# Optimization experiments

Hardware: AMD Instinct MI355X
Metric: run time of the kernel (lower is better)

## Reference

```python
import jax, jax.numpy as jnp
import numpy as np

BS, N, HID = 16384, 16, 512  # batch, n coords (state dim = 2n), mlp hidden


def setup_inputs() -> dict:
    key = jax.random.key(0)
    ks = jax.random.split(key, 4)
    d = 2 * N
    x = jax.random.normal(ks[0], (BS, d), dtype=jnp.float32)
    # Lagrangian MLP: 2n -> HID -> HID -> 1 with softplus (smooth 2nd derivs)
    W1 = jax.random.normal(ks[1], (d, HID), dtype=jnp.float32) / np.sqrt(d)
    b1 = jnp.zeros((HID,), jnp.float32)
    W2 = jax.random.normal(ks[2], (HID, HID), dtype=jnp.float32) / np.sqrt(HID)
    b2 = jnp.zeros((HID,), jnp.float32)
    W3 = jax.random.normal(ks[3], (HID, 1), dtype=jnp.float32) / np.sqrt(HID)
    b3 = jnp.zeros((1,), jnp.float32)
    return {"x": x, "W1": W1, "b1": b1, "W2": W2, "b2": b2, "W3": W3, "b3": b3}


def reference(x, W1, b1, W2, b2, W3, b3):
    n = x.shape[1] // 2

    def lagrangian(qqd):  # qqd: [2n] -> scalar
        h = jax.nn.softplus(qqd @ W1 + b1)
        h = jax.nn.softplus(h @ W2 + b2)
        return jnp.sum(h @ W3 + b3)

    # batched first derivative (jacobian of scalar) and hessian; replaces the
    # per-sample python loop of torch.autograd.functional.jacobian/hessian
    jac = jax.vmap(jax.grad(lagrangian))(x)          # [bs, 2n]
    hess = jax.vmap(jax.hessian(lagrangian))(x)      # [bs, 2n, 2n]

    qd = x[:, n:]                                    # [bs, n]
    A = hess[:, n:, n:]                              # d2L/dqd dqd  [bs, n, n]
    B = hess[:, n:, :n]                              # d2L/dqd dq   [bs, n, n]
    rhs = jac[:, :n] - jnp.einsum('bij,bj->bi', B, qd)  # [bs, n]
    qdd = jnp.einsum('bij,bj->bi', jnp.linalg.pinv(A), rhs)  # [bs, n]
    return jnp.concatenate([qd, qdd], axis=1)        # [bs, 2n]
```

## Files before the change

### kernel.cpp

```cpp
#include <hip/hip_runtime.h>
#include <math.h>


#define NSWEEP 5
#define JAX_RCOND 1.9073486e-5

typedef unsigned int uint;
typedef unsigned short ushort;
typedef float f2 __attribute__((ext_vector_type(2)));
typedef float f4 __attribute__((ext_vector_type(4)));
typedef short bf16x8 __attribute__((ext_vector_type(8)));
typedef float f32x16 __attribute__((ext_vector_type(16)));
typedef uint uint2v __attribute__((ext_vector_type(2)));

#define OFF_R    0
#define R_FLOATS 12288
#define OFF_S1   12288
#define OFF_H1   13312
#define OFF_G2   14336
#define OFF_D2   15360
#define OFF_U    16384
#define OFF_X    17408
#define OFF_JAC  17472
#define OFF_T1   17504
#define OFF_T2   18560
#define OFF_AUG  19616
#define SMEM_FLOATS 20160
#define SMEM_BYTES  (SMEM_FLOATS*4)

#define SOLVE_WAVE_DBL 592
#define SOLVE_SMEM_BYTES (4*SOLVE_WAVE_DBL*8)

#define PACK_BYTES 524288

__device__ __forceinline__ ushort f2bf(float x) {
    uint u = __float_as_uint(x);
    return (ushort)((u + 0x7fffu + ((u >> 16) & 1u)) >> 16);
}
__device__ __forceinline__ float bf2f(ushort h) {
    return __uint_as_float(((uint)h) << 16);
}
__device__ __forceinline__ void split3(float x, ushort& h, ushort& m, ushort& l) {
    h = f2bf(x); float r1 = x - bf2f(h);
    m = f2bf(r1); float r2 = r1 - bf2f(m);
    l = f2bf(r2);
}

__device__ __forceinline__ void pairpq(int r, int m, int& p, int& q) {
    p = (m == 0) ? 0 : 1 + (m - 1 + r) % 15;
    q = 1 + (14 - m + r) % 15;
}

__device__ __forceinline__ void wave_fence() {
    __builtin_amdgcn_wave_barrier();
    __builtin_amdgcn_s_waitcnt(0);
    __builtin_amdgcn_wave_barrier();
}

__device__ __forceinline__ void jacobi_solve_wave(
    const float* __restrict__ gaug, double* __restrict__ ws,
    float* __restrict__ outp, int lane)
{
    double* Ad  = ws;
    double* Vd  = Ad + 272;
    double* c8  = Vd + 272;
    double* sn8 = c8 + 8;
    double* il  = sn8 + 8;
    double* yv  = il + 16;

    for (int idx = lane; idx < 272; idx += 64) {
        const int r = idx / 17, c = idx - r*17;
        double a = 0.0;
        if (c < 16) a = 0.5 * ((double)gaug[r*17 + c] + (double)gaug[c*17 + r]);
        Ad[idx] = a;
        Vd[idx] = (c < 16 && r == c) ? 1.0 : 0.0;
    }
    wave_fence();

    for (int sweep = 0; sweep < NSWEEP; ++sweep) {
        for (int rr = 0; rr < 15; ++rr) {
            if (lane < 8) {
                int p, q; pairpq(rr, lane, p, q);
                const double app = Ad[p*17 + p], aqq = Ad[q*17 + q], apq = Ad[p*17 + q];
                double cc = 1.0, ss = 0.0;
                if (apq != 0.0) {
                    const double tau = (aqq - app) / (2.0 * apq);
                    const double tt = ((tau >= 0.0) ? 1.0 : -1.0) / (fabs(tau) + sqrt(1.0 + tau*tau));
                    cc = 1.0 / sqrt(1.0 + tt*tt);
                    ss = tt * cc;
                }
                c8[lane] = cc; sn8[lane] = ss;
            }
            wave_fence();
            #pragma unroll
            for (int k = 0; k < 2; ++k) {
                const int id = lane + 64*k;
                const int m = id >> 4, j = id & 15;
                int p, q; pairpq(rr, m, p, q);
                const double cc = c8[m], ss = sn8[m];
                const double ap = Ad[p*17 + j], aq = Ad[q*17 + j];
                Ad[p*17 + j] = cc*ap - ss*aq;
                Ad[q*17 + j] = ss*ap + cc*aq;
            }
            #pragma unroll
            for (int k = 0; k < 2; ++k) {
                const int id = lane + 64*k;
                const int m = id >> 4, i = id & 15;
                int p, q; pairpq(rr, m, p, q);
                const double cc = c8[m], ss = sn8[m];
                const double vp = Vd[i*17 + p], vq = Vd[i*17 + q];
                Vd[i*17 + p] = cc*vp - ss*vq;
                Vd[i*17 + q] = ss*vp + cc*vq;
            }
            wave_fence();
            #pragma unroll
            for (int k = 0; k < 2; ++k) {
                const int id = lane + 64*k;
                const int m = id >> 4, i = id & 15;
                int p, q; pairpq(rr, m, p, q);
                const double cc = c8[m], ss = sn8[m];
                const double ap = Ad[i*17 + p], aq = Ad[i*17 + q];
                Ad[i*17 + p] = cc*ap - ss*aq;
                Ad[i*17 + q] = ss*ap + cc*aq;
            }
            wave_fence();
        }
    }

    if (lane == 0) {
        double mx = 0.0;
        #pragma unroll
        for (int i = 0; i < 16; ++i) mx = fmax(mx, fabs(Ad[i*17 + i]));
        const double cut = JAX_RCOND * mx;
        #pragma unroll
        for (int i = 0; i < 16; ++i) {
            const double l = Ad[i*17 + i];
            il[i] = (fabs(l) > cut) ? (1.0 / l) : 0.0;
        }
    }
    wave_fence();

    if (lane < 16) {
        double a = 0.0;
        #pragma unroll
        for (int r = 0; r < 16; ++r) a += Vd[r*17 + lane] * (double)gaug[r*17 + 16];
        yv[lane] = a;
    }
    wave_fence();

    if (lane < 16) {
        double a = 0.0;
        #pragma unroll
        for (int i = 0; i < 16; ++i) a += Vd[lane*17 + i] * (il[i] * yv[i]);
        outp[lane] = (float)a;
    }
}

extern "C" __global__ void w1_transpose(const float* __restrict__ W1,
                                        float* __restrict__ W1T) {
    const int t = blockIdx.x * 256 + threadIdx.x;
    W1T[t] = W1[(t & 31) * 512 + (t >> 5)];
}

extern "C" __global__ void w2_pack(const float* __restrict__ W2,
                                   uint* __restrict__ pHi,
                                   uint* __restrict__ pMid,
                                   uint* __restrict__ pLo) {
    const int tid = blockIdx.x * 256 + threadIdx.x;
    const int lane = tid & 63;
    const int k0 = ((tid >> 6) & 31) * 16 + (lane >> 5) * 8;
    const int n  = (tid >> 11) * 32 + (lane & 31);
    uint h[4], m[4], l[4];
    #pragma unroll
    for (int e2 = 0; e2 < 4; ++e2) {
        ushort h0, m0, l0, h1, m1, l1;
        split3(W2[(k0 + 2*e2    )*512 + n], h0, m0, l0);
        split3(W2[(k0 + 2*e2 + 1)*512 + n], h1, m1, l1);
        h[e2] = (uint)h0 | ((uint)h1 << 16);
        m[e2] = (uint)m0 | ((uint)m1 << 16);
        l[e2] = (uint)l0 | ((uint)l1 << 16);
    }
    #pragma unroll
    for (int e2 = 0; e2 < 4; ++e2) {
        pHi [tid*4 + e2] = h[e2];
        pMid[tid*4 + e2] = m[e2];
        pLo [tid*4 + e2] = l[e2];
    }
}

#define MFMA32(A, B, C) __builtin_amdgcn_mfma_f32_32x32x16_bf16((A), (B), (C), 0, 0, 0)

extern "C" __global__ __launch_bounds__(256, 2)
void lnn_kernel(const float* __restrict__ x,
                const float* __restrict__ W1,
                const float* __restrict__ W1T,
                const float* __restrict__ b1,
                const float* __restrict__ W2, const float* __restrict__ b2,
                const float* __restrict__ W3,
                float* __restrict__ out,
                float* __restrict__ aug_g,
                const uint* __restrict__ pHi,
                const uint* __restrict__ pMid,
                const uint* __restrict__ pLo,
                const int solveInMain)
{
    const int b0 = blockIdx.x * 2;
    const int t = threadIdx.x;
    const int lane = t & 63;
    const int w = t >> 6;

    extern __shared__ float sm[];
    char*  A8    = (char*)sm;
    float* s_ws  = sm + OFF_R;
    char*  Mq8   = (char*)sm;
    float* s_s1  = sm + OFF_S1;
    float* s_h1  = sm + OFF_H1;
    float* s_g2  = sm + OFF_G2;
    float* s_d2  = sm + OFF_D2;
    float* s_u   = sm + OFF_U;
    float* s_x   = sm + OFF_X;
    float* s_jac = sm + OFF_JAC;
    float* s_T1  = sm + OFF_T1;
    float* s_T2  = sm + OFF_T2;
    float* s_aug = sm + OFF_AUG;

    if (t < 64) s_x[t] = x[b0*32 + t];
    if (t < 32) {
        const int s = t >> 4, i = t & 15;
        out[(b0+s)*32 + i] = x[(b0+s)*32 + 16 + i];
    }
    __syncthreads();

    #pragma unroll
    for (int rep = 0; rep < 4; ++rep) {
        const int s = rep >> 1;
        const int j = t + (rep & 1)*256;
        float z = b1[j];
        const f4* wt = (const f4*)(W1T + j*32);
        const float* xs = s_x + s*32;
        #pragma unroll
        for (int i4 = 0; i4 < 8; ++i4) {
            const f4 wv = wt[i4];
            z = fmaf(xs[i4*4 + 0], wv.x, z);
            z = fmaf(xs[i4*4 + 1], wv.y, z);
            z = fmaf(xs[i4*4 + 2], wv.z, z);
            z = fmaf(xs[i4*4 + 3], wv.w, z);
        }
        const float e = expf(-fabsf(z));
        const float sg = (z >= 0.f) ? 1.f/(1.f+e) : e/(1.f+e);
        s_s1[s*512 + j] = sg;
        s_h1[s*512 + j] = fmaxf(z, 0.f) + log1pf(e);
    }
    __syncthreads();

    {
        const int c = w*128 + lane*2;
        const f2 bz = *(const f2*)(b2 + c);
        float za[2][2] = { {bz.x, bz.y}, {bz.x, bz.y} };
        #pragma unroll 8
        for (int j = 0; j < 512; ++j) {
            const f2 wv = *(const f2*)(W2 + j*512 + c);
            const float h0 = s_h1[j];
            const float h1 = s_h1[512 + j];
            za[0][0] = fmaf(h0, wv.x, za[0][0]);
            za[0][1] = fmaf(h0, wv.y, za[0][1]);
            za[1][0] = fmaf(h1, wv.x, za[1][0]);
            za[1][1] = fmaf(h1, wv.y, za[1][1]);
        }
        const f2 w3v = *(const f2*)(W3 + c);
        #pragma unroll
        for (int s = 0; s < 2; ++s) {
            const float e0 = expf(-fabsf(za[s][0]));
            const float sg0 = (za[s][0] >= 0.f) ? 1.f/(1.f+e0) : e0/(1.f+e0);
            const float e1v = expf(-fabsf(za[s][1]));
            const float sg1 = (za[s][1] >= 0.f) ? 1.f/(1.f+e1v) : e1v/(1.f+e1v);
            f2 g2v = { w3v.x * sg0, w3v.y * sg1 };
            f2 d2v = { w3v.x * sg0 * (1.f - sg0), w3v.y * sg1 * (1.f - sg1) };
            *(f2*)(s_g2 + s*512 + c) = g2v;
            *(f2*)(s_d2 + s*512 + c) = d2v;
        }
    }
    __syncthreads();

    {
        float g2a[8], g2b[8];
        {
            const float4 ga = *(const float4*)(s_g2 + lane*8);
            const float4 gb = *(const float4*)(s_g2 + lane*8 + 4);
            g2a[0]=ga.x; g2a[1]=ga.y; g2a[2]=ga.z; g2a[3]=ga.w;
            g2a[4]=gb.x; g2a[5]=gb.y; g2a[6]=gb.z; g2a[7]=gb.w;
            const float4 gc = *(const float4*)(s_g2 + 512 + lane*8);
            const float4 gd = *(const float4*)(s_g2 + 512 + lane*8 + 4);
            g2b[0]=gc.x; g2b[1]=gc.y; g2b[2]=gc.z; g2b[3]=gc.w;
            g2b[4]=gd.x; g2b[5]=gd.y; g2b[6]=gd.z; g2b[7]=gd.w;
        }
        for (int jj = 0; jj < 32; ++jj) {
            float pr0[4], pr1[4];
            #pragma unroll
            for (int s4 = 0; s4 < 4; ++s4) {
                const int j = w*128 + jj + s4*32;
                const float4 ra = *(const float4*)(W2 + j*512 + lane*8);
                const float4 rb = *(const float4*)(W2 + j*512 + lane*8 + 4);
                float p0 = ra.x*g2a[0];
                p0 = fmaf(ra.y, g2a[1], p0); p0 = fmaf(ra.z, g2a[2], p0); p0 = fmaf(ra.w, g2a[3], p0);
                p0 = fmaf(rb.x, g2a[4], p0); p0 = fmaf(rb.y, g2a[5], p0);
                p0 = fmaf(rb.z, g2a[6], p0); p0 = fmaf(rb.w, g2a[7], p0);
                pr0[s4] = p0;
                float p1 = ra.x*g2b[0];
                p1 = fmaf(ra.y, g2b[1], p1); p1 = fmaf(ra.z, g2b[2], p1); p1 = fmaf(ra.w, g2b[3], p1);
                p1 = fmaf(rb.x, g2b[4], p1); p1 = fmaf(rb.y, g2b[5], p1);
                p1 = fmaf(rb.z, g2b[6], p1); p1 = fmaf(rb.w, g2b[7], p1);
                pr1[s4] = p1;
            }
            #pragma unroll
            for (int off = 32; off >= 1; off >>= 1) {
                #pragma unroll
                for (int s4 = 0; s4 < 4; ++s4) {
                    pr0[s4] += __shfl_xor(pr0[s4], off);
                    pr1[s4] += __shfl_xor(pr1[s4], off);
                }
            }
            if (lane == 0) {
                #pragma unroll
                for (int s4 = 0; s4 < 4; ++s4) {
                    s_u[w*128 + jj + s4*32]       = pr0[s4];
                    s_u[512 + w*128 + jj + s4*32] = pr1[s4];
                }
            }
        }
    }
    __syncthreads();

    #pragma unroll
    for (int rep = 0; rep < 4; ++rep) {
        const int j = (rep >> 1)*512 + t + (rep & 1)*256;
        const float uj = s_u[j], sv = s_s1[j];
        s_h1[j] = uj * (1.f - sv) / sv;
    }

    const int i5 = 16 + (t >> 4);
    const int c5 = 2 * (t & 15);

    {
        const f4* W1Tv4 = (const f4*)W1T;
        float jacp[2] = {0.f, 0.f};
        float t1a[2] = {0.f, 0.f}, t1b[2] = {0.f, 0.f};

        for (int q = 0; q < 4; ++q) {
            __syncthreads();
            #pragma unroll
            for (int r = 0; r < 4; ++r) {
                const int f = r*256 + t;
                const f4 wv = W1Tv4[q*1024 + f];
                #pragma unroll
                for (int s = 0; s < 2; ++s) {
                    const float sv = s_s1[s*512 + q*128 + (f >> 3)];
                    f4 v = wv;
                    v.x*=sv; v.y*=sv; v.z*=sv; v.w*=sv;
                    ((f4*)(s_ws + s*4096))[f] = v;
                }
            }
            __syncthreads();

            if (w == q) {
                const int i  = t & 15;
                const int jb = (lane >> 4) * 32;
                #pragma unroll
                for (int s = 0; s < 2; ++s) {
                    const float* wsp = s_ws + s*4096;
                    const float* up  = s_u + s*512 + q*128;
                    float jp = jacp[s];
                    #pragma unroll 8
                    for (int jj = 0; jj < 32; ++jj)
                        jp = fmaf(wsp[(jb+jj)*32 + i], up[jb + jj], jp);
                    jacp[s] = jp;
                }
            }

            #pragma unroll
            for (int s = 0; s < 2; ++s) {
                const float* wsp = s_ws + s*4096;
                const float* ep  = s_h1 + s*512 + q*128;
                float a = t1a[s], bv = t1b[s];
                #pragma unroll 4
                for (int jj = 0; jj < 128; ++jj) {
                    const float e   = ep[jj];
                    const float wsi = wsp[jj*32 + i5];
                    const f2 wc = *(const f2*)(wsp + jj*32 + c5);
                    const float tt  = wsi * e;
                    a  = fmaf(tt, wc.x, a);
                    bv = fmaf(tt, wc.y, bv);
                }
                t1a[s] = a; t1b[s] = bv;
            }
        }
        #pragma unroll
        for (int s = 0; s < 2; ++s) {
            s_T1[s*528 + (i5-16)*33 + c5]     = t1a[s];
            s_T1[s*528 + (i5-16)*33 + c5 + 1] = t1b[s];
            s_g2[s*512 + (t>>4)*16 + (t&15)]  = jacp[s];
        }
    }
    __syncthreads();

    if (t < 32) {
        const int s = t >> 4, i = t & 15;
        float p = 0.f;
        #pragma unroll
        for (int seg = 0; seg < 16; ++seg) p += s_g2[s*512 + seg*16 + i];
        s_jac[s*16 + i] = p;
    }

    float h0acc[2] = {0.f, 0.f}, h1acc[2] = {0.f, 0.f};
    {
        const f4* W1v4 = (const f4*)W1;
        const f4* s1v4 = (const f4*)s_s1;
        const bf16x8* pHiV  = (const bf16x8*)pHi;
        const bf16x8* pMidV = (const bf16x8*)pMid;
        const bf16x8* pLoV  = (const bf16x8*)pLo;
        const int arow = lane & 31;
        const uint abase = (uint)arow * 256u;
        const uint aswz = (uint)(arow & 15);
        const int rowadd = 4 * (lane >> 5);
        const int cl = lane & 31;
        const uint swi = (uint)((i5 >> 1) & 7);
        const uint swc = (uint)((c5 >> 1) & 7);

        #pragma unroll 1
        for (int half = 0; half < 2; ++half) {
            f32x16 acc00{}, acc01{}, acc10{}, acc11{};
            const int NT0 = 2*half, NT1 = 2*half + 1;

            #pragma unroll 1
            for (int q = 0; q < 4; ++q) {
                __syncthreads();
                #pragma unroll
                for (int r = 0; r < 4; ++r) {
                    const int f = r*256 + t;
                    const int i = f >> 5, k4 = f & 31;
                    const f4 wv = W1v4[i*128 + q*32 + k4];
                    const uint off = (uint)i*256u + (((uint)k4*8u) ^ (((uint)(i & 15)) << 4));
                    #pragma unroll
                    for (int s = 0; s < 2; ++s) {
                        const f4 sv = s1v4[s*128 + q*32 + k4];
                        ushort h[4], m[4], l[4];
                        split3(wv.x*sv.x, h[0], m[0], l[0]);
                        split3(wv.y*sv.y, h[1], m[1], l[1]);
                        split3(wv.z*sv.z, h[2], m[2], l[2]);
                        split3(wv.w*sv.w, h[3], m[3], l[3]);
                        uint2v vh = { (uint)h[0] | ((uint)h[1]<<16), (uint)h[2] | ((uint)h[3]<<16) };
                        uint2v vm = { (uint)m[0] | ((uint)m[1]<<16), (uint)m[2] | ((uint)m[3]<<16) };
                        uint2v vl = { (uint)l[0] | ((uint)l[1]<<16), (uint)l[2] | ((uint)l[3]<<16) };
                        char* base = A8 + s*24576;
                        *(uint2v*)(base + off)         = vh;
                        *(uint2v*)(base + 8192 + off)  = vm;
                        *(uint2v*)(base + 16384 + off) = vl;
                    }
                }
                __syncthreads();

                #pragma unroll 2
                for (int ks8 = 0; ks8 < 8; ++ks8) {
                    const uint slot = (uint)(ks8*2 + (lane >> 5));
                    const uint aoff = abase + ((slot ^ aswz) << 4);
                    const bf16x8 aHi0  = *(const bf16x8*)(A8 + aoff);
                    const bf16x8 aMid0 = *(const bf16x8*)(A8 + 8192 + aoff);
                    const bf16x8 aLo0  = *(const bf16x8*)(A8 + 16384 + aoff);
                    const bf16x8 aHi1  = *(const bf16x8*)(A8 + 24576 + aoff);
                    const bf16x8 aMid1 = *(const bf16x8*)(A8 + 24576 + 8192 + aoff);
                    const bf16x8 aLo1  = *(const bf16x8*)(A8 + 24576 + 16384 + aoff);
                    const int pbase = (w*128 + q*8 + ks8)*64 + lane;
                    #define KSTEP(A0, A1, NT) { \
                        const bf16x8 bHi  = pHiV [pbase + (NT)*2048]; \
                        const bf16x8 bMid = pMidV[pbase + (NT)*2048]; \
                        const bf16x8 bLo  = pLoV [pbase + (NT)*2048]; \
                        A0 = MFMA32(aHi0,  bHi,  A0); \
                        A0 = MFMA32(aHi0,  bMid, A0); \
                        A0 = MFMA32(aMid0, bHi,  A0); \
                        A0 = MFMA32(aMid0, bMid, A0); \
                        A0 = MFMA32(aHi0,  bLo,  A0); \
                        A0 = MFMA32(aLo0,  bHi,  A0); \
                        A1 = MFMA32(aHi1,  bHi,  A1); \
                        A1 = MFMA32(aHi1,  bMid, A1); \
                        A1 = MFMA32(aMid1, bHi,  A1); \
                        A1 = MFMA32(aMid1, bMid, A1); \
                        A1 = MFMA32(aHi1,  bLo,  A1); \
                        A1 = MFMA32(aLo1,  bHi,  A1); }
                    KSTEP(acc00, acc10, NT0)
                    KSTEP(acc01, acc11, NT1)
                    #undef KSTEP
                }
            }
            __syncthreads();

            for (int p = 0; p < 4; ++p) {
                if (w == p) {
                    #define WRFRAG(ACC, SOFF, NT) { \
                        _Pragma("unroll") \
                        for (int r = 0; r < 16; ++r) { \
                            const int row = (r & 3) + 8*(r >> 2) + rowadd; \
                            const int col = (NT)*32 + cl; \
                            const uint slot = ((uint)(col >> 2)) ^ ((uint)((row >> 1) & 7)); \
                            *(float*)(Mq8 + (SOFF) + row*528 + (slot << 4) + ((col & 3) << 2)) = ACC[r]; \
                        } }
                    WRFRAG(acc00, 0, NT0)
                    WRFRAG(acc01, 0, NT1)
                    WRFRAG(acc10, 16896, NT0)
                    WRFRAG(acc11, 16896, NT1)
                    #undef WRFRAG
                }
                __syncthreads();
                #pragma unroll
                for (int s = 0; s < 2; ++s) {
                    const f4* d2q = (const f4*)(s_d2 + s*512);
                    const char* MiB = Mq8 + s*16896 + i5*528;
                    const char* MaB = Mq8 + s*16896 + c5*528;
                    const char* MbB = Mq8 + s*16896 + (c5+1)*528;
                    float h0 = h0acc[s], h1v = h1acc[s];
                    for (int qq = half*16; qq < half*16 + 16; ++qq) {
                        const f4 d  = d2q[p*32 + qq];
                        const f4 mi = *(const f4*)(MiB + (((uint)qq ^ swi) << 4));
                        const f4 ma = *(const f4*)(MaB + (((uint)qq ^ swc) << 4));
                        const f4 mb = *(const f4*)(MbB + (((uint)qq ^ swc) << 4));
                        float tt;
                        tt = mi.x*d.x; h0 = fmaf(tt, ma.x, h0); h1v = fmaf(tt, mb.x, h1v);
                        tt = mi.y*d.y; h0 = fmaf(tt, ma.y, h0); h1v = fmaf(tt, mb.y, h1v);
                        tt = mi.z*d.z; h0 = fmaf(tt, ma.z, h0); h1v = fmaf(tt, mb.z, h1v);
                        tt = mi.w*d.w; h0 = fmaf(tt, ma.w, h0); h1v = fmaf(tt, mb.w, h1v);
                    }
                    h0acc[s] = h0; h1acc[s] = h1v;
                }
                __syncthreads();
            }
        }
        #pragma unroll
        for (int s = 0; s < 2; ++s) {
            s_T2[s*528 + (i5-16)*33 + c5]     = h0acc[s];
            s_T2[s*528 + (i5-16)*33 + c5 + 1] = h1acc[s];
        }
    }
    __syncthreads();

    {
        const int r = t >> 4, c = t & 15;
        #pragma unroll
        for (int s = 0; s < 2; ++s)
            s_aug[s*272 + r*17 + c] = s_T1[s*528 + r*33 + 16 + c] + s_T2[s*528 + r*33 + 16 + c];
    }
    if (t < 32) {
        const int s = t >> 4, i = t & 15;
        float p = s_jac[s*16 + i];
        #pragma unroll
        for (int c = 0; c < 16; ++c)
            p -= (s_T1[s*528 + i*33 + c] + s_T2[s*528 + i*33 + c]) * s_x[s*32 + 16 + c];
        s_aug[s*272 + i*17 + 16] = p;
    }
    __syncthreads();

    if (!solveInMain) {
        aug_g[b0*272 + t]       = s_aug[t];
        aug_g[b0*272 + 256 + t] = s_aug[256 + t];
        if (t < 32) aug_g[b0*272 + 512 + t] = s_aug[512 + t];
        return;
    }

    if (w >= 2) return;
    jacobi_solve_wave(s_aug + w*272, (double*)sm + w*SOLVE_WAVE_DBL,
                      out + (b0+w)*32 + 16, lane);
}

extern "C" __global__ __launch_bounds__(256, 8)
void lnn_solve(const float* __restrict__ aug_g, float* __restrict__ out)
{
    const int t = threadIdx.x;
    const int lane = t & 63;
    const int w = t >> 6;
    const int b = blockIdx.x * 4 + w;

    extern __shared__ double dsm[];
    jacobi_solve_wave(aug_g + b*272, dsm + w*SOLVE_WAVE_DBL, out + b*32 + 16, lane);
}

extern "C" void kernel_launch(void* const* d_in, const int* in_sizes, int n_in,
                              void* d_out, int out_size, void* d_ws, size_t ws_size,
                              hipStream_t stream) {
    const float* x  = (const float*)d_in[0];
    const float* W1 = (const float*)d_in[1];
    const float* b1 = (const float*)d_in[2];
    const float* W2 = (const float*)d_in[3];
    const float* b2 = (const float*)d_in[4];
    const float* W3 = (const float*)d_in[5];
    float* out = (float*)d_out;

    float* W1T = (float*)d_ws;
    uint*  pHi  = (uint*)((char*)d_ws + 65536);
    uint*  pMid = (uint*)((char*)d_ws + 65536 + PACK_BYTES);
    uint*  pLo  = (uint*)((char*)d_ws + 65536 + 2*PACK_BYTES);
    float* aug  = (float*)((char*)d_ws + 65536 + 3*PACK_BYTES);
    const int bs = in_sizes[0] / 32;

    const size_t need = 65536 + 3*(size_t)PACK_BYTES + (size_t)bs * 272 * 4;
    const int solveInMain = (ws_size < need) ? 1 : 0;

    hipFuncSetAttribute((const void*)lnn_kernel,
                        hipFuncAttributeMaxDynamicSharedMemorySize, SMEM_BYTES);
    w1_transpose<<<dim3(64), dim3(256), 0, stream>>>(W1, W1T);
    w2_pack<<<dim3(128), dim3(256), 0, stream>>>(W2, pHi, pMid, pLo);
    lnn_kernel<<<dim3(bs/2), dim3(256), SMEM_BYTES, stream>>>(
        x, W1, W1T, b1, W2, b2, W3, out, aug, pHi, pMid, pLo, solveInMain);
    if (!solveInMain)
        lnn_solve<<<dim3(bs/4), dim3(256), SOLVE_SMEM_BYTES, stream>>>(aug, out);
}
```

Measured before the change: 3.360 ms.

## Fuse layer-2 forward GEMV into the MFMA W2 pass via split-bf16 operands

Removes the separate fp32 scalar loop over W2 that computed the layer-2 pre-activations. Instead, h1 for both samples is split into three bf16 parts in shared memory and fed as an extra A operand to the MFMA loop that already streams the W2 fragments, producing z2 alongside the Hessian accumulators. The backward u pass and the T1/jac computation are moved after the MFMA stage, since g2 and d2 now come out of it. This reuses W2 loads but adds 24 MFMAs per k-step (mostly wasted rows in the 32-row tile), drops unrolling of the k loop to 1, and raises register pressure.

```diff
diff --git a/kernel.cpp b/kernel.cpp
--- a/kernel.cpp
+++ b/kernel.cpp
@@ -223,6 +223,8 @@
     float* s_T1  = sm + OFF_T1;
     float* s_T2  = sm + OFF_T2;
     float* s_aug = sm + OFF_AUG;
+    char*  zB   = (char*)s_u;
+    char*  zLoB = (char*)s_h1;
 
     if (t < 64) s_x[t] = x[b0*32 + t];
     if (t < 32) {
@@ -254,162 +256,22 @@
     __syncthreads();
 
     {
-        const int c = w*128 + lane*2;
-        const f2 bz = *(const f2*)(b2 + c);
-        float za[2][2] = { {bz.x, bz.y}, {bz.x, bz.y} };
-        #pragma unroll 8
-        for (int j = 0; j < 512; ++j) {
-            const f2 wv = *(const f2*)(W2 + j*512 + c);
-            const float h0 = s_h1[j];
-            const float h1 = s_h1[512 + j];
-            za[0][0] = fmaf(h0, wv.x, za[0][0]);
-            za[0][1] = fmaf(h0, wv.y, za[0][1]);
-            za[1][0] = fmaf(h1, wv.x, za[1][0]);
-            za[1][1] = fmaf(h1, wv.y, za[1][1]);
-        }
-        const f2 w3v = *(const f2*)(W3 + c);
-        #pragma unroll
-        for (int s = 0; s < 2; ++s) {
-            const float e0 = expf(-fabsf(za[s][0]));
-            const float sg0 = (za[s][0] >= 0.f) ? 1.f/(1.f+e0) : e0/(1.f+e0);
-            const float e1v = expf(-fabsf(za[s][1]));
-            const float sg1 = (za[s][1] >= 0.f) ? 1.f/(1.f+e1v) : e1v/(1.f+e1v);
-            f2 g2v = { w3v.x * sg0, w3v.y * sg1 };
-            f2 d2v = { w3v.x * sg0 * (1.f - sg0), w3v.y * sg1 * (1.f - sg1) };
-            *(f2*)(s_g2 + s*512 + c) = g2v;
-            *(f2*)(s_d2 + s*512 + c) = d2v;
-        }
-    }
-    __syncthreads();
-
-    {
-        float g2a[8], g2b[8];
-        {
-            const float4 ga = *(const float4*)(s_g2 + lane*8);
-            const float4 gb = *(const float4*)(s_g2 + lane*8 + 4);
-            g2a[0]=ga.x; g2a[1]=ga.y; g2a[2]=ga.z; g2a[3]=ga.w;
-            g2a[4]=gb.x; g2a[5]=gb.y; g2a[6]=gb.z; g2a[7]=gb.w;
-            const float4 gc = *(const float4*)(s_g2 + 512 + lane*8);
-            const float4 gd = *(const float4*)(s_g2 + 512 + lane*8 + 4);
-            g2b[0]=gc.x; g2b[1]=gc.y; g2b[2]=gc.z; g2b[3]=gc.w;
-            g2b[4]=gd.x; g2b[5]=gd.y; g2b[6]=gd.z; g2b[7]=gd.w;
-        }
-        for (int jj = 0; jj < 32; ++jj) {
-            float pr0[4], pr1[4];
-            #pragma unroll
-            for (int s4 = 0; s4 < 4; ++s4) {
-                const int j = w*128 + jj + s4*32;
-                const float4 ra = *(const float4*)(W2 + j*512 + lane*8);
-                const float4 rb = *(const float4*)(W2 + j*512 + lane*8 + 4);
-                float p0 = ra.x*g2a[0];
-                p0 = fmaf(ra.y, g2a[1], p0); p0 = fmaf(ra.z, g2a[2], p0); p0 = fmaf(ra.w, g2a[3], p0);
-                p0 = fmaf(rb.x, g2a[4], p0); p0 = fmaf(rb.y, g2a[5], p0);
-                p0 = fmaf(rb.z, g2a[6], p0); p0 = fmaf(rb.w, g2a[7], p0);
-                pr0[s4] = p0;
-                float p1 = ra.x*g2b[0];
-                p1 = fmaf(ra.y, g2b[1], p1); p1 = fmaf(ra.z, g2b[2], p1); p1 = fmaf(ra.w, g2b[3], p1);
-                p1 = fmaf(rb.x, g2b[4], p1); p1 = fmaf(rb.y, g2b[5], p1);
-                p1 = fmaf(rb.z, g2b[6], p1); p1 = fmaf(rb.w, g2b[7], p1);
-                pr1[s4] = p1;
-            }
-            #pragma unroll
-            for (int off = 32; off >= 1; off >>= 1) {
-                #pragma unroll
-                for (int s4 = 0; s4 < 4; ++s4) {
-                    pr0[s4] += __shfl_xor(pr0[s4], off);
-                    pr1[s4] += __shfl_xor(pr1[s4], off);
-                }
-            }
-            if (lane == 0) {
-                #pragma unroll
-                for (int s4 = 0; s4 < 4; ++s4) {
-                    s_u[w*128 + jj + s4*32]       = pr0[s4];
-                    s_u[512 + w*128 + jj + s4*32] = pr1[s4];
-                }
-            }
-        }
-    }
-    __syncthreads();
-
-    #pragma unroll
-    for (int rep = 0; rep < 4; ++rep) {
-        const int j = (rep >> 1)*512 + t + (rep & 1)*256;
-        const float uj = s_u[j], sv = s_s1[j];
-        s_h1[j] = uj * (1.f - sv) / sv;
+        const float a0 = s_h1[2*t],       c0v = s_h1[2*t + 1];
+        const float a1 = s_h1[512 + 2*t], c1v = s_h1[512 + 2*t + 1];
+        __syncthreads();
+        ushort ha, ma, la, hc, mc, lc;
+        split3(a0, ha, ma, la); split3(c0v, hc, mc, lc);
+        ((uint*)(zB + 0))[t]    = (uint)ha | ((uint)hc << 16);
+        ((uint*)(zB + 2048))[t] = (uint)ma | ((uint)mc << 16);
+        ((uint*)(zLoB + 0))[t]  = (uint)la | ((uint)lc << 16);
+        split3(a1, ha, ma, la); split3(c1v, hc, mc, lc);
+        ((uint*)(zB + 1024))[t] = (uint)ha | ((uint)hc << 16);
+        ((uint*)(zB + 3072))[t] = (uint)ma | ((uint)mc << 16);
+        ((uint*)(zLoB + 1024))[t] = (uint)la | ((uint)lc << 16);
     }
 
     const int i5 = 16 + (t >> 4);
     const int c5 = 2 * (t & 15);
-
-    {
-        const f4* W1Tv4 = (const f4*)W1T;
-        float jacp[2] = {0.f, 0.f};
-        float t1a[2] = {0.f, 0.f}, t1b[2] = {0.f, 0.f};
-
-        for (int q = 0; q < 4; ++q) {
-            __syncthreads();
-            #pragma unroll
-            for (int r = 0; r < 4; ++r) {
-                const int f = r*256 + t;
-                const f4 wv = W1Tv4[q*1024 + f];
-                #pragma unroll
-                for (int s = 0; s < 2; ++s) {
-                    const float sv = s_s1[s*512 + q*128 + (f >> 3)];
-                    f4 v = wv;
-                    v.x*=sv; v.y*=sv; v.z*=sv; v.w*=sv;
-                    ((f4*)(s_ws + s*4096))[f] = v;
-                }
-            }
-            __syncthreads();
-
-            if (w == q) {
-                const int i  = t & 15;
-                const int jb = (lane >> 4) * 32;
-                #pragma unroll
-                for (int s = 0; s < 2; ++s) {
-                    const float* wsp = s_ws + s*4096;
-                    const float* up  = s_u + s*512 + q*128;
-                    float jp = jacp[s];
-                    #pragma unroll 8
-                    for (int jj = 0; jj < 32; ++jj)
-                        jp = fmaf(wsp[(jb+jj)*32 + i], up[jb + jj], jp);
-                    jacp[s] = jp;
-                }
-            }
-
-            #pragma unroll
-            for (int s = 0; s < 2; ++s) {
-                const float* wsp = s_ws + s*4096;
-                const float* ep  = s_h1 + s*512 + q*128;
-                float a = t1a[s], bv = t1b[s];
-                #pragma unroll 4
-                for (int jj = 0; jj < 128; ++jj) {
-                    const float e   = ep[jj];
-                    const float wsi = wsp[jj*32 + i5];
-                    const f2 wc = *(const f2*)(wsp + jj*32 + c5);
-                    const float tt  = wsi * e;
-                    a  = fmaf(tt, wc.x, a);
-                    bv = fmaf(tt, wc.y, bv);
-                }
-                t1a[s] = a; t1b[s] = bv;
-            }
-        }
-        #pragma unroll
-        for (int s = 0; s < 2; ++s) {
-            s_T1[s*528 + (i5-16)*33 + c5]     = t1a[s];
-            s_T1[s*528 + (i5-16)*33 + c5 + 1] = t1b[s];
-            s_g2[s*512 + (t>>4)*16 + (t&15)]  = jacp[s];
-        }
-    }
-    __syncthreads();
-
-    if (t < 32) {
-        const int s = t >> 4, i = t & 15;
-        float p = 0.f;
-        #pragma unroll
-        for (int seg = 0; seg < 16; ++seg) p += s_g2[s*512 + seg*16 + i];
-        s_jac[s*16 + i] = p;
-    }
 
     float h0acc[2] = {0.f, 0.f}, h1acc[2] = {0.f, 0.f};
     {
@@ -421,6 +283,7 @@
         const int arow = lane & 31;
         const uint abase = (uint)arow * 256u;
         const uint aswz = (uint)(arow & 15);
+        const uint kbyte = (uint)((lane >> 5) << 4);
         const int rowadd = 4 * (lane >> 5);
         const int cl = lane & 31;
         const uint swi = (uint)((i5 >> 1) & 7);
@@ -429,6 +292,7 @@
         #pragma unroll 1
         for (int half = 0; half < 2; ++half) {
             f32x16 acc00{}, acc01{}, acc10{}, acc11{};
+            f32x16 az00{}, az01{}, az10{}, az11{};
             const int NT0 = 2*half, NT1 = 2*half + 1;
 
             #pragma unroll 1
@@ -459,7 +323,7 @@
                 }
                 __syncthreads();
 
-                #pragma unroll 2
+                #pragma unroll 1
                 for (int ks8 = 0; ks8 < 8; ++ks8) {
                     const uint slot = (uint)(ks8*2 + (lane >> 5));
                     const uint aoff = abase + ((slot ^ aswz) << 4);
@@ -469,8 +333,15 @@
                     const bf16x8 aHi1  = *(const bf16x8*)(A8 + 24576 + aoff);
                     const bf16x8 aMid1 = *(const bf16x8*)(A8 + 24576 + 8192 + aoff);
                     const bf16x8 aLo1  = *(const bf16x8*)(A8 + 24576 + 16384 + aoff);
+                    const uint zoff = (uint)(q*256 + ks8*32) + kbyte;
+                    const bf16x8 zHi0  = *(const bf16x8*)(zB + zoff);
+                    const bf16x8 zHi1  = *(const bf16x8*)(zB + 1024 + zoff);
+                    const bf16x8 zMid0 = *(const bf16x8*)(zB + 2048 + zoff);
+                    const bf16x8 zMid1 = *(const bf16x8*)(zB + 3072 + zoff);
+                    const bf16x8 zLo0  = *(const bf16x8*)(zLoB + zoff);
+                    const bf16x8 zLo1  = *(const bf16x8*)(zLoB + 1024 + zoff);
                     const int pbase = (w*128 + q*8 + ks8)*64 + lane;
-                    #define KSTEP(A0, A1, NT) { \
+                    #define KSTEP(A0, A1, Z0, Z1, NT) { \
                         const bf16x8 bHi  = pHiV [pbase + (NT)*2048]; \
                         const bf16x8 bMid = pMidV[pbase + (NT)*2048]; \
                         const bf16x8 bLo  = pLoV [pbase + (NT)*2048]; \
@@ -485,10 +356,53 @@
                         A1 = MFMA32(aMid1, bHi,  A1); \
                         A1 = MFMA32(aMid1, bMid, A1); \
                         A1 = MFMA32(aHi1,  bLo,  A1); \
-                        A1 = MFMA32(aLo1,  bHi,  A1); }
-                    KSTEP(acc00, acc10, NT0)
-                    KSTEP(acc01, acc11, NT1)
+                        A1 = MFMA32(aLo1,  bHi,  A1); \
+                        Z0 = MFMA32(zHi0,  bHi,  Z0); \
+                        Z0 = MFMA32(zHi0,  bMid, Z0); \
+                        Z0 = MFMA32(zMid0, bHi,  Z0); \
+                        Z0 = MFMA32(zMid0, bMid, Z0); \
+                        Z0 = MFMA32(zHi0,  bLo,  Z0); \
+                        Z0 = MFMA32(zLo0,  bHi,  Z0); \
+                        Z1 = MFMA32(zHi1,  bHi,  Z1); \
+                        Z1 = MFMA32(zHi1,  bMid, Z1); \
+                        Z1 = MFMA32(zMid1, bHi,  Z1); \
+                        Z1 = MFMA32(zMid1, bMid, Z1); \
+                        Z1 = MFMA32(zHi1,  bLo,  Z1); \
+                        Z1 = MFMA32(zLo1,  bHi,  Z1); }
+                    KSTEP(acc00, acc10, az00, az10, NT0)
+                    KSTEP(acc01, acc11, az01, az11, NT1)
                     #undef KSTEP
+                }
+            }
+
+            if (lane < 32) {
+                const int c0g = w*128 + NT0*32 + lane;
+                const int c1g = c0g + 32;
+                const float bz0 = b2[c0g], bz1 = b2[c1g];
+                const float w30 = W3[c0g], w31 = W3[c1g];
+                {
+                    const float z0 = az00[0] + bz0;
+                    const float z1 = az01[0] + bz1;
+                    const float e0 = expf(-fabsf(z0));
+                    const float sg0 = (z0 >= 0.f) ? 1.f/(1.f+e0) : e0/(1.f+e0);
+                    const float e1v = expf(-fabsf(z1));
+                    const float sg1 = (z1 >= 0.f) ? 1.f/(1.f+e1v) : e1v/(1.f+e1v);
+                    s_g2[c0g] = w30 * sg0;
+                    s_d2[c0g] = w30 * sg0 * (1.f - sg0);
+                    s_g2[c1g] = w31 * sg1;
+                    s_d2[c1g] = w31 * sg1 * (1.f - sg1);
+                }
+                {
+                    const float z0 = az10[0] + bz0;
+                    const float z1 = az11[0] + bz1;
+                    const float e0 = expf(-fabsf(z0));
+                    const float sg0 = (z0 >= 0.f) ? 1.f/(1.f+e0) : e0/(1.f+e0);
+                    const float e1v = expf(-fabsf(z1));
+                    const float sg1 = (z1 >= 0.f) ? 1.f/(1.f+e1v) : e1v/(1.f+e1v);
+                    s_g2[512 + c0g] = w30 * sg0;
+                    s_d2[512 + c0g] = w30 * sg0 * (1.f - sg0);
+                    s_g2[512 + c1g] = w31 * sg1;
+                    s_d2[512 + c1g] = w31 * sg1 * (1.f - sg1);
                 }
             }
             __syncthreads();
@@ -542,11 +456,138 @@
     __syncthreads();
 
     {
+        float g2a[8], g2b[8];
+        {
+            const float4 ga = *(const float4*)(s_g2 + lane*8);
+            const float4 gb = *(const float4*)(s_g2 + lane*8 + 4);
+            g2a[0]=ga.x; g2a[1]=ga.y; g2a[2]=ga.z; g2a[3]=ga.w;
+            g2a[4]=gb.x; g2a[5]=gb.y; g2a[6]=gb.z; g2a[7]=gb.w;
+            const float4 gc = *(const float4*)(s_g2 + 512 + lane*8);
+            const float4 gd = *(const float4*)(s_g2 + 512 + lane*8 + 4);
+            g2b[0]=gc.x; g2b[1]=gc.y; g2b[2]=gc.z; g2b[3]=gc.w;
+            g2b[4]=gd.x; g2b[5]=gd.y; g2b[6]=gd.z; g2b[7]=gd.w;
+        }
+        for (int jj = 0; jj < 32; ++jj) {
+            float pr0[4], pr1[4];
+            #pragma unroll
+            for (int s4 = 0; s4 < 4; ++s4) {
+                const int j = w*128 + jj + s4*32;
+                const float4 ra = *(const float4*)(W2 + j*512 + lane*8);
+                const float4 rb = *(const float4*)(W2 + j*512 + lane*8 + 4);
+                float p0 = ra.x*g2a[0];
+                p0 = fmaf(ra.y, g2a[1], p0); p0 = fmaf(ra.z, g2a[2], p0); p0 = fmaf(ra.w, g2a[3], p0);
+                p0 = fmaf(rb.x, g2a[4], p0); p0 = fmaf(rb.y, g2a[5], p0);
+                p0 = fmaf(rb.z, g2a[6], p0); p0 = fmaf(rb.w, g2a[7], p0);
+                pr0[s4] = p0;
+                float p1 = ra.x*g2b[0];
+                p1 = fmaf(ra.y, g2b[1], p1); p1 = fmaf(ra.z, g2b[2], p1); p1 = fmaf(ra.w, g2b[3], p1);
+                p1 = fmaf(rb.x, g2b[4], p1); p1 = fmaf(rb.y, g2b[5], p1);
+                p1 = fmaf(rb.z, g2b[6], p1); p1 = fmaf(rb.w, g2b[7], p1);
+                pr1[s4] = p1;
+            }
+            #pragma unroll
+            for (int off = 32; off >= 1; off >>= 1) {
+                #pragma unroll
+                for (int s4 = 0; s4 < 4; ++s4) {
+                    pr0[s4] += __shfl_xor(pr0[s4], off);
+                    pr1[s4] += __shfl_xor(pr1[s4], off);
+                }
+            }
+            if (lane == 0) {
+                #pragma unroll
+                for (int s4 = 0; s4 < 4; ++s4) {
+                    s_u[w*128 + jj + s4*32]       = pr0[s4];
+                    s_u[512 + w*128 + jj + s4*32] = pr1[s4];
+                }
+            }
+        }
+    }
+    __syncthreads();
+
+    #pragma unroll
+    for (int rep = 0; rep < 4; ++rep) {
+        const int j = (rep >> 1)*512 + t + (rep & 1)*256;
+        const float uj = s_u[j], sv = s_s1[j];
+        s_h1[j] = uj * (1.f - sv) / sv;
+    }
+
+    {
+        const f4* W1Tv4 = (const f4*)W1T;
+        float jacp[2] = {0.f, 0.f};
+        float t1a[2] = {0.f, 0.f}, t1b[2] = {0.f, 0.f};
+
+        for (int q = 0; q < 4; ++q) {
+            __syncthreads();
+            #pragma unroll
+            for (int r = 0; r < 4; ++r) {
+                const int f = r*256 + t;
+                const f4 wv = W1Tv4[q*1024 + f];
+                #pragma unroll
+                for (int s = 0; s < 2; ++s) {
+                    const float sv = s_s1[s*512 + q*128 + (f >> 3)];
+                    f4 v = wv;
+                    v.x*=sv; v.y*=sv; v.z*=sv; v.w*=sv;
+                    ((f4*)(s_ws + s*4096))[f] = v;
+                }
+            }
+            __syncthreads();
+
+            if (w == q) {
+                const int i  = t & 15;
+                const int jb = (lane >> 4) * 32;
+                #pragma unroll
+                for (int s = 0; s < 2; ++s) {
+                    const float* wsp = s_ws + s*4096;
+                    const float* up  = s_u + s*512 + q*128;
+                    float jp = jacp[s];
+                    #pragma unroll 8
+                    for (int jj = 0; jj < 32; ++jj)
+                        jp = fmaf(wsp[(jb+jj)*32 + i], up[jb + jj], jp);
+                    jacp[s] = jp;
+                }
+            }
+
+            #pragma unroll
+            for (int s = 0; s < 2; ++s) {
+                const float* wsp = s_ws + s*4096;
+                const float* ep  = s_h1 + s*512 + q*128;
+                float a = t1a[s], bv = t1b[s];
+                #pragma unroll 4
+                for (int jj = 0; jj < 128; ++jj) {
+                    const float e   = ep[jj];
+                    const float wsi = wsp[jj*32 + i5];
+                    const f2 wc = *(const f2*)(wsp + jj*32 + c5);
+                    const float tt  = wsi * e;
+                    a  = fmaf(tt, wc.x, a);
+                    bv = fmaf(tt, wc.y, bv);
+                }
+                t1a[s] = a; t1b[s] = bv;
+            }
+        }
+        #pragma unroll
+        for (int s = 0; s < 2; ++s) {
+            s_T1[s*528 + (i5-16)*33 + c5]     = t1a[s];
+            s_T1[s*528 + (i5-16)*33 + c5 + 1] = t1b[s];
+            s_g2[s*512 + (t>>4)*16 + (t&15)]  = jacp[s];
+        }
+    }
+    __syncthreads();
+
+    if (t < 32) {
+        const int s = t >> 4, i = t & 15;
+        float p = 0.f;
+        #pragma unroll
+        for (int seg = 0; seg < 16; ++seg) p += s_g2[s*512 + seg*16 + i];
+        s_jac[s*16 + i] = p;
+    }
+    {
         const int r = t >> 4, c = t & 15;
         #pragma unroll
         for (int s = 0; s < 2; ++s)
             s_aug[s*272 + r*17 + c] = s_T1[s*528 + r*33 + 16 + c] + s_T2[s*528 + r*33 + 16 + c];
     }
+    __syncthreads();
+
     if (t < 32) {
         const int s = t >> 4, i = t & 15;
         float p = s_jac[s*16 + i];
```

Measured after the change: 4.097 ms. 1.22x slower.
